# Optimization experiments

Hardware: AMD Instinct MI355X
Metric: run time of the kernel (lower is better)

Reference implementation:

```python
import jax, jax.numpy as jnp
import numpy as np
from jax import lax

B, C, H, W = 4, 64, 128, 128
G, K, RED = 16, 7, 4        # groups, kernel size, reduce ratio
CR = C // RED               # reduced channels for kernel generation
EPS = 1e-5                  # BatchNorm eps (torch default)
DN = ('NCHW', 'OIHW', 'NCHW')


def setup_inputs() -> dict:
    key = jax.random.key(0)
    ks = jax.random.split(key, 5)
    return {
        'input': jax.random.normal(ks[0], (B, C, H, W), jnp.float32),
        # initial_mapping: depthwise 3x3 conv + pointwise 1x1 conv (bias=False)
        'w_dw': jax.random.normal(ks[1], (C, 1, 3, 3), jnp.float32) * 0.1,
        'w_pw': jax.random.normal(ks[2], (C, C), jnp.float32) * (1.0 / np.sqrt(C)),
        # sigma_mapping BatchNorm affine params
        'bn_gamma': jnp.ones((CR,), jnp.float32),
        'bn_beta': jnp.zeros((CR,), jnp.float32),
        # reduce / span 1x1 convs (bias=False)
        'w_reduce': jax.random.normal(ks[3], (CR, C), jnp.float32) * (1.0 / np.sqrt(C)),
        'w_span': jax.random.normal(ks[4], (K * K * G, CR), jnp.float32) * (1.0 / np.sqrt(CR)),
    }


def reference(input, w_dw, w_pw, bn_gamma, bn_beta, w_reduce, w_span):
    x = input
    # initial mapping: depthwise 3x3 (pad 1) then 1x1 pointwise
    h = lax.conv_general_dilated(x, w_dw, (1, 1), [(1, 1), (1, 1)],
                                 feature_group_count=C, dimension_numbers=DN)
    h = jnp.einsum('bchw,oc->bohw', h, w_pw)
    # unfold -> [B, C*K*K, H, W] with channel-major feature ordering (matches torch Unfold)
    patches = lax.conv_general_dilated_patches(h, (K, K), (1, 1), [(3, 3), (3, 3)],
                                               dimension_numbers=DN)
    patches = patches.reshape(B, G, C // G, K * K, H, W)
    # kernel generation: o_mapping is identity (stride 1 avg pool), then reduce -> BN(train) -> ReLU -> span
    r = jnp.einsum('bchw,oc->bohw', x, w_reduce)           # [B, CR, H, W]
    mean = r.mean(axis=(0, 2, 3), keepdims=True)
    var = r.var(axis=(0, 2, 3), keepdims=True)             # biased var, as torch BN training
    r = (r - mean) * lax.rsqrt(var + EPS) * bn_gamma[None, :, None, None] + bn_beta[None, :, None, None]
    r = jax.nn.relu(r)
    kern = jnp.einsum('bchw,oc->bohw', r, w_span)          # [B, G*K*K, H, W]
    kern = kern.reshape(B, G, 1, K * K, H, W)
    out = (kern * patches).sum(axis=3)                     # [B, G, C//G, H, W]
    return out.reshape(B, C, H, W)
```

## Files before the change

### kernel.cpp

```cpp
#include <hip/hip_runtime.h>

typedef _Float16 half2v __attribute__((ext_vector_type(2)));
typedef _Float16 half4v __attribute__((ext_vector_type(4)));
typedef _Float16 half8v __attribute__((ext_vector_type(8)));
typedef float f32x4 __attribute__((ext_vector_type(4)));

__launch_bounds__(256, 4)
__global__ void k_front(const float* __restrict__ in, const float* __restrict__ wdw,
                        const float* __restrict__ wpw, const float* __restrict__ wred,
                        _Float16* __restrict__ h16, _Float16* __restrict__ r16,
                        float* __restrict__ partial){
  __shared__ float4 s_in4[4][10][12];
  __shared__ __attribute__((aligned(16))) _Float16 s_dwh[64][72];
  __shared__ __attribute__((aligned(16))) _Float16 s_cvh[64][72];
  __shared__ float s_red[4][32];
  int t = threadIdx.x;
  int w = t >> 6, lane = t & 63;
  int lx = lane & 7, ly = lane >> 3;
  int c15 = lane & 15, hi = lane >> 4;
  int blk0 = blockIdx.x;

  int blk = ((blk0 & 7) << 7) | (blk0 >> 3);
  int tile = blk & 255, b = blk >> 8;
  int x0 = (tile & 15) << 3, y0 = (tile >> 4) << 3;
  const float* inb = in + ((long)b << 20) + ((long)(w << 2) << 14);

  int p1 = lane + 64;
  int ry0 = lane / 10, rx0 = lane - ry0 * 10;
  int ry1 = p1 / 10,   rx1 = p1 - ry1 * 10;
  int yy0 = y0 + ry0 - 1, xx0 = x0 + rx0 - 1;
  int yy1 = y0 + ry1 - 1, xx1 = x0 + rx1 - 1;
  bool ok0 = (unsigned)yy0 < 128u && (unsigned)xx0 < 128u;
  bool ok1 = (p1 < 100) && ((unsigned)yy1 < 128u) && ((unsigned)xx1 < 128u);
  int o0 = (yy0 << 7) + xx0, o1 = (yy1 << 7) + xx1;

  float4 vb0[4], vb1[4];
  #pragma unroll
  for (int q = 0; q < 4; q++){
    const float* pq = inb + ((long)q << 18);
    float4 a = make_float4(0.f,0.f,0.f,0.f), bb = a;
    if (ok0){ a.x  = pq[o0]; a.y  = pq[o0+16384]; a.z  = pq[o0+32768]; a.w  = pq[o0+49152]; }
    if (ok1){ bb.x = pq[o1]; bb.y = pq[o1+16384]; bb.z = pq[o1+32768]; bb.w = pq[o1+49152]; }
    vb0[q] = a; vb1[q] = bb;
  }

  const float* ap = wpw + (((w << 4) + c15) << 6) + (hi << 3);
  float4 ap0 = *(const float4*)(ap);
  float4 ap1 = *(const float4*)(ap + 4);
  float4 ap2 = *(const float4*)(ap + 32);
  float4 ap3 = *(const float4*)(ap + 36);
  const float* arp = wred + (c15 << 6) + (hi << 3);
  float4 ar0 = *(const float4*)(arp);
  float4 ar1 = *(const float4*)(arp + 4);
  float4 ar2 = *(const float4*)(arp + 32);
  float4 ar3 = *(const float4*)(arp + 36);
  half8v a_pw0 = {(_Float16)ap0.x,(_Float16)ap0.y,(_Float16)ap0.z,(_Float16)ap0.w,
                  (_Float16)ap1.x,(_Float16)ap1.y,(_Float16)ap1.z,(_Float16)ap1.w};
  half8v a_pw1 = {(_Float16)ap2.x,(_Float16)ap2.y,(_Float16)ap2.z,(_Float16)ap2.w,
                  (_Float16)ap3.x,(_Float16)ap3.y,(_Float16)ap3.z,(_Float16)ap3.w};
  half8v a_rd0 = {(_Float16)ar0.x,(_Float16)ar0.y,(_Float16)ar0.z,(_Float16)ar0.w,
                  (_Float16)ar1.x,(_Float16)ar1.y,(_Float16)ar1.z,(_Float16)ar1.w};
  half8v a_rd1 = {(_Float16)ar2.x,(_Float16)ar2.y,(_Float16)ar2.z,(_Float16)ar2.w,
                  (_Float16)ar3.x,(_Float16)ar3.y,(_Float16)ar3.z,(_Float16)ar3.w};

  #pragma unroll
  for (int q = 0; q < 4; q++){
    s_in4[w][ry0][rx0] = vb0[q];
    if (p1 < 100) s_in4[w][ry1][rx1] = vb1[q];
    __builtin_amdgcn_wave_barrier();

    int wdbase = __builtin_amdgcn_readfirstlane(((q << 4) + (w << 2)) * 9);
    const float* wd = wdw + wdbase;
    float4 a = make_float4(0.f,0.f,0.f,0.f);
    float4 cv = make_float4(0.f,0.f,0.f,0.f);
    #pragma unroll
    for (int dy = 0; dy < 3; dy++){
      #pragma unroll
      for (int dx = 0; dx < 3; dx++){
        float4 v = s_in4[w][ly + dy][lx + dx];
        int k = dy * 3 + dx;
        a.x += v.x * wd[k];
        a.y += v.y * wd[9 + k];
        a.z += v.z * wd[18 + k];
        a.w += v.w * wd[27 + k];
        if (k == 4) cv = v;
      }
    }
    int cb = (q << 4) + (w << 2);
    half4v ah = {(_Float16)a.x,(_Float16)a.y,(_Float16)a.z,(_Float16)a.w};
    half4v eh = {(_Float16)cv.x,(_Float16)cv.y,(_Float16)cv.z,(_Float16)cv.w};
    *(half4v*)&s_dwh[lane][cb] = ah;
    *(half4v*)&s_cvh[lane][cb] = eh;
    __builtin_amdgcn_wave_barrier();
  }

  __syncthreads();

  f32x4 z = {0.f,0.f,0.f,0.f};
  f32x4 acc[4] = {z, z, z, z};
  #pragma unroll
  for (int tt = 0; tt < 4; tt++){
    half8v b0 = *(const half8v*)&s_dwh[(tt << 4) + c15][hi << 3];
    half8v b1 = *(const half8v*)&s_dwh[(tt << 4) + c15][32 + (hi << 3)];
    acc[tt] = __builtin_amdgcn_mfma_f32_16x16x32_f16(a_pw0, b0, acc[tt], 0, 0, 0);
    acc[tt] = __builtin_amdgcn_mfma_f32_16x16x32_f16(a_pw1, b1, acc[tt], 0, 0, 0);
  }
  #pragma unroll
  for (int tt = 0; tt < 4; tt++){
    int px = (tt << 4) + c15;
    int pyl = px >> 3, pxl = px & 7;
    int gout = (w << 2) + hi;
    long off = ((((long)((b << 4) + gout)) << 14) + ((y0 + pyl) << 7) + x0 + pxl) << 2;
    half4v hv = {(_Float16)acc[tt][0], (_Float16)acc[tt][1],
                 (_Float16)acc[tt][2], (_Float16)acc[tt][3]};
    *(half4v*)&h16[off] = hv;
  }

  f32x4 rac = z;
  {
    half8v b0 = *(const half8v*)&s_cvh[(w << 4) + c15][hi << 3];
    half8v b1 = *(const half8v*)&s_cvh[(w << 4) + c15][32 + (hi << 3)];
    rac = __builtin_amdgcn_mfma_f32_16x16x32_f16(a_rd0, b0, rac, 0, 0, 0);
    rac = __builtin_amdgcn_mfma_f32_16x16x32_f16(a_rd1, b1, rac, 0, 0, 0);
  }
  {
    int px = (w << 4) + c15;
    int pyl = px >> 3, pxl = px & 7;
    long roff = ((((long)b << 14) + ((y0 + pyl) << 7) + x0 + pxl) << 4) + (hi << 2);
    half4v rv4 = {(_Float16)rac[0], (_Float16)rac[1], (_Float16)rac[2], (_Float16)rac[3]};
    *(half4v*)&r16[roff] = rv4;
  }

  #pragma unroll
  for (int rr = 0; rr < 4; rr++){
    float v = rac[rr], s2 = v * v;
    #pragma unroll
    for (int m = 1; m < 16; m <<= 1){
      v  += __shfl_xor(v,  m, 64);
      s2 += __shfl_xor(s2, m, 64);
    }
    if (c15 == 0){
      int ch = (hi << 2) + rr;
      s_red[w][2 * ch]     = v;
      s_red[w][2 * ch + 1] = s2;
    }
  }
  __syncthreads();
  if (t < 32)
    partial[(blk0 << 5) + t] = s_red[0][t] + s_red[1][t] + s_red[2][t] + s_red[3][t];
}

__global__ void k_red(const float* __restrict__ partial, const float* __restrict__ gamma,
                      const float* __restrict__ beta, float* __restrict__ sb,
                      const float* __restrict__ wspan, _Float16* __restrict__ w16){
  __shared__ float sp[1024];
  int t = threadIdx.x;
  int c = t & 31, grp = t >> 5;
  float s = 0.f;
  #pragma unroll 4
  for (int i = grp; i < 1024; i += 32) s += partial[(i << 5) + c];
  sp[t] = s;
  for (int i = t; i < 12544; i += 1024) w16[i] = (_Float16)wspan[i];
  __syncthreads();
  if (t < 32){
    float v = 0.f;
    #pragma unroll
    for (int k = 0; k < 32; k++) v += sp[(k << 5) + t];
    sp[t] = v;
  }
  __syncthreads();
  if (t < 16){
    const float inv_n = 1.52587890625e-5f;
    float mean = sp[2 * t] * inv_n;
    float var  = sp[2 * t + 1] * inv_n - mean * mean;
    float inv  = rsqrtf(var + 1e-5f);
    float sc   = gamma[t] * inv;
    sb[2 * t]     = sc;
    sb[2 * t + 1] = beta[t] - mean * sc;
  }
}

__launch_bounds__(64, 4)
__global__ void k_main(const _Float16* __restrict__ h16, const _Float16* __restrict__ r16,
                       const float* __restrict__ sb, const _Float16* __restrict__ w16,
                       float* __restrict__ out){
  __shared__ float4 s_h4[14][15];
  int lane = threadIdx.x;
  int g = blockIdx.y, b = blockIdx.z;
  int bx = blockIdx.x;
  bx = ((bx & 7) << 5) | (bx >> 3);
  int tx0 = (bx & 15) << 3, ty0 = (bx >> 4) << 3;
  int ltx = lane & 7, lty = lane >> 3;
  int px = tx0 + ltx, py = ty0 + lty;

  const _Float16* rp = r16 + ((((long)b << 14) + (py << 7) + px) << 4);
  half8v ra = *(const half8v*)rp;
  half8v rb = *(const half8v*)(rp + 8);

  const _Float16* hp = h16 + (((long)((b << 4) + g)) << 16);
  #pragma unroll
  for (int i = 0; i < 4; i++){
    int p = lane + (i << 6);
    if (p < 196){
      int ry = p / 14, rx = p - ry * 14;
      int yy = ty0 + ry - 3, xx = tx0 + rx - 3;
      float4 v = make_float4(0.f,0.f,0.f,0.f);
      if ((unsigned)yy < 128u && (unsigned)xx < 128u){
        half4v hh = *(const half4v*)&hp[(long)(((yy << 7) + xx) << 2)];
        v = make_float4((float)hh[0], (float)hh[1], (float)hh[2], (float)hh[3]);
      }
      s_h4[ry][rx] = v;
    }
  }
  __builtin_amdgcn_wave_barrier();

  float rv[16];
  #pragma unroll
  for (int c = 0; c < 8; c++){
    rv[c]     = fmaxf((float)ra[c] * sb[2*c]     + sb[2*c+1],     0.f);
    rv[c + 8] = fmaxf((float)rb[c] * sb[2*(c+8)] + sb[2*(c+8)+1], 0.f);
  }
#if __has_builtin(__builtin_amdgcn_fdot2)
  half2v rv2[8];
  #pragma unroll
  for (int j = 0; j < 8; j++){
    half2v pk; pk[0] = (_Float16)rv[2*j]; pk[1] = (_Float16)rv[2*j+1];
    rv2[j] = pk;
  }
#endif

  const _Float16* wg = w16 + g * 784;
#if __has_builtin(__builtin_amdgcn_fdot2)
  const half2v* wg2 = (const half2v*)wg;
#endif
  float acc0 = 0.f, acc1 = 0.f, acc2 = 0.f, acc3 = 0.f;
  #pragma unroll
  for (int kh = 0; kh < 7; kh++){
    #pragma unroll
    for (int kw = 0; kw < 7; kw++){
      int k = kh * 7 + kw;
      float kv0 = 0.f, kv1 = 0.f;
#if __has_builtin(__builtin_amdgcn_fdot2)
      #pragma unroll
      for (int j = 0; j < 4; j++){
        kv0 = __builtin_amdgcn_fdot2(rv2[j],     wg2[k*8 + j],     kv0, false);
        kv1 = __builtin_amdgcn_fdot2(rv2[j + 4], wg2[k*8 + j + 4], kv1, false);
      }
#else
      #pragma unroll
      for (int c = 0; c < 8; c++){
        kv0 += rv[c]     * (float)wg[k*16 + c];
        kv1 += rv[c + 8] * (float)wg[k*16 + c + 8];
      }
#endif
      float kv = kv0 + kv1;
      float4 hv = s_h4[lty + kh][ltx + kw];
      acc0 += kv * hv.x;
      acc1 += kv * hv.y;
      acc2 += kv * hv.z;
      acc3 += kv * hv.w;
    }
  }

  long obase = (((long)((b << 6) + (g << 2))) << 14) + (py << 7) + px;
  out[obase]         = acc0;
  out[obase + 16384] = acc1;
  out[obase + 32768] = acc2;
  out[obase + 49152] = acc3;
}

extern "C" void kernel_launch(void* const* d_in, const int* in_sizes, int n_in,
                              void* d_out, int out_size, void* d_ws, size_t ws_size,
                              hipStream_t stream){
  const float* in       = (const float*)d_in[0];
  const float* w_dw     = (const float*)d_in[1];
  const float* w_pw     = (const float*)d_in[2];
  const float* gamma    = (const float*)d_in[3];
  const float* beta     = (const float*)d_in[4];
  const float* w_reduce = (const float*)d_in[5];
  const float* w_span   = (const float*)d_in[6];
  float* out = (float*)d_out;

  _Float16* h16 = (_Float16*)d_ws;
  _Float16* r16 = h16 + 4194304;
  _Float16* w16 = r16 + 1048576;
  float* partial = (float*)(w16 + 16384);
  float* sb      = partial + 32768;

  k_front<<<1024, 256, 0, stream>>>(in, w_dw, w_pw, w_reduce, h16, r16, partial);
  k_red  <<<1, 1024, 0, stream>>>(partial, gamma, beta, sb, w_span, w16);
  dim3 grid(256, 16, 4);
  k_main <<<grid, 64, 0, stream>>>(h16, r16, sb, w16, out);
}
```

Baseline: 121.5 us.

## Replace reduction kernel with atomics and fold BN finalize into main kernel

Removes the single-block k_red kernel. k_front now accumulates the BN sum and sum-of-squares into a 32-float stats buffer with atomicAdd, and also converts w_span to fp16. k_main recomputes scale and bias from the stats in every block and keeps them in shared memory. This saves one serialized single-block launch, but adds a memset, 32K float atomics contending on 32 addresses, and a redundant per-block finalize. It also makes the float summation order nondeterministic.

```diff
diff --git a/kernel.cpp b/kernel.cpp
--- a/kernel.cpp
+++ b/kernel.cpp
@@ -8,8 +8,9 @@
 __launch_bounds__(256, 4)
 __global__ void k_front(const float* __restrict__ in, const float* __restrict__ wdw,
                         const float* __restrict__ wpw, const float* __restrict__ wred,
+                        const float* __restrict__ wspan,
                         _Float16* __restrict__ h16, _Float16* __restrict__ r16,
-                        float* __restrict__ partial){
+                        float* __restrict__ stats, _Float16* __restrict__ w16){
   __shared__ float4 s_in4[4][10][12];
   __shared__ __attribute__((aligned(16))) _Float16 s_dwh[64][72];
   __shared__ __attribute__((aligned(16))) _Float16 s_cvh[64][72];
@@ -19,6 +20,11 @@
   int lx = lane & 7, ly = lane >> 3;
   int c15 = lane & 15, hi = lane >> 4;
   int blk0 = blockIdx.x;
+
+  {
+    int i = blk0 * 256 + t;
+    if (i < 12544) w16[i] = (_Float16)wspan[i];
+  }
 
   int blk = ((blk0 & 7) << 7) | (blk0 >> 3);
   int tile = blk & 255, b = blk >> 8;
@@ -146,45 +152,19 @@
     }
   }
   __syncthreads();
-  if (t < 32)
-    partial[(blk0 << 5) + t] = s_red[0][t] + s_red[1][t] + s_red[2][t] + s_red[3][t];
-}
-
-__global__ void k_red(const float* __restrict__ partial, const float* __restrict__ gamma,
-                      const float* __restrict__ beta, float* __restrict__ sb,
-                      const float* __restrict__ wspan, _Float16* __restrict__ w16){
-  __shared__ float sp[1024];
-  int t = threadIdx.x;
-  int c = t & 31, grp = t >> 5;
-  float s = 0.f;
-  #pragma unroll 4
-  for (int i = grp; i < 1024; i += 32) s += partial[(i << 5) + c];
-  sp[t] = s;
-  for (int i = t; i < 12544; i += 1024) w16[i] = (_Float16)wspan[i];
-  __syncthreads();
   if (t < 32){
-    float v = 0.f;
-    #pragma unroll
-    for (int k = 0; k < 32; k++) v += sp[(k << 5) + t];
-    sp[t] = v;
-  }
-  __syncthreads();
-  if (t < 16){
-    const float inv_n = 1.52587890625e-5f;
-    float mean = sp[2 * t] * inv_n;
-    float var  = sp[2 * t + 1] * inv_n - mean * mean;
-    float inv  = rsqrtf(var + 1e-5f);
-    float sc   = gamma[t] * inv;
-    sb[2 * t]     = sc;
-    sb[2 * t + 1] = beta[t] - mean * sc;
+    float sum = s_red[0][t] + s_red[1][t] + s_red[2][t] + s_red[3][t];
+    atomicAdd(&stats[t], sum);
   }
 }
 
 __launch_bounds__(64, 4)
 __global__ void k_main(const _Float16* __restrict__ h16, const _Float16* __restrict__ r16,
-                       const float* __restrict__ sb, const _Float16* __restrict__ w16,
+                       const float* __restrict__ stats, const float* __restrict__ gamma,
+                       const float* __restrict__ beta, const _Float16* __restrict__ w16,
                        float* __restrict__ out){
   __shared__ float4 s_h4[14][15];
+  __shared__ float  s_sb[32];
   int lane = threadIdx.x;
   int g = blockIdx.y, b = blockIdx.z;
   int bx = blockIdx.x;
@@ -212,13 +192,23 @@
       s_h4[ry][rx] = v;
     }
   }
+
+  if (lane < 16){
+    const float inv_n = 1.52587890625e-5f;
+    float mean = stats[2 * lane] * inv_n;
+    float var  = stats[2 * lane + 1] * inv_n - mean * mean;
+    float inv  = rsqrtf(var + 1e-5f);
+    float sc   = gamma[lane] * inv;
+    s_sb[2 * lane]     = sc;
+    s_sb[2 * lane + 1] = beta[lane] - mean * sc;
+  }
   __builtin_amdgcn_wave_barrier();
 
   float rv[16];
   #pragma unroll
   for (int c = 0; c < 8; c++){
-    rv[c]     = fmaxf((float)ra[c] * sb[2*c]     + sb[2*c+1],     0.f);
-    rv[c + 8] = fmaxf((float)rb[c] * sb[2*(c+8)] + sb[2*(c+8)+1], 0.f);
+    rv[c]     = fmaxf((float)ra[c] * s_sb[2*c]     + s_sb[2*c+1],     0.f);
+    rv[c + 8] = fmaxf((float)rb[c] * s_sb[2*(c+8)] + s_sb[2*(c+8)+1], 0.f);
   }
 #if __has_builtin(__builtin_amdgcn_fdot2)
   half2v rv2[8];
@@ -284,11 +274,11 @@
   _Float16* h16 = (_Float16*)d_ws;
   _Float16* r16 = h16 + 4194304;
   _Float16* w16 = r16 + 1048576;
-  float* partial = (float*)(w16 + 16384);
-  float* sb      = partial + 32768;
-
-  k_front<<<1024, 256, 0, stream>>>(in, w_dw, w_pw, w_reduce, h16, r16, partial);
-  k_red  <<<1, 1024, 0, stream>>>(partial, gamma, beta, sb, w_span, w16);
+  float* stats  = (float*)(w16 + 16384);
+
+  hipMemsetAsync(stats, 0, 32 * sizeof(float), stream);
+  k_front<<<1024, 256, 0, stream>>>(in, w_dw, w_pw, w_reduce, w_span,
+                                    h16, r16, stats, w16);
   dim3 grid(256, 16, 4);
-  k_main <<<grid, 64, 0, stream>>>(h16, r16, sb, w16, out);
+  k_main <<<grid, 64, 0, stream>>>(h16, r16, stats, gamma, beta, w16, out);
 }
```

New measurement: 126.1 us. 3.8% more time.
